# Kernel optimization log

Measured on AMD Instinct MI355X. Metric: run time of the kernel, lower is better.

## Reference

```python
import jax, jax.numpy as jnp
import numpy as np

B, L, D, H = 8, 1024, 512, 8
DH = D // H  # 64
EPS = 1e-5


def setup_inputs() -> dict:
    key = jax.random.key(0)
    ks = jax.random.split(key, 9)
    query = jax.random.normal(ks[0], (B, L, D), dtype=jnp.float32)
    key_t = jax.random.normal(ks[1], (B, L, D), dtype=jnp.float32)
    value = jax.random.normal(ks[2], (B, L, D), dtype=jnp.float32)
    attn_mask = jax.random.bernoulli(ks[3], 0.1, (B, L, L))
    softmax_mask = jax.random.bernoulli(ks[4], 0.1, (B, L, L))
    s = 1.0 / np.sqrt(D)
    Wq = jax.random.uniform(ks[5], (D, D), jnp.float32, -s, s)
    Wk = jax.random.uniform(ks[6], (D, D), jnp.float32, -s, s)
    Wv = jax.random.uniform(ks[7], (D, D), jnp.float32, -s, s)
    Wo = jax.random.uniform(ks[8], (D, D), jnp.float32, -s, s)
    return {"query": query, "key": key_t, "value": value,
            "attn_mask": attn_mask, "softmax_mask": softmax_mask,
            "Wq": Wq, "Wk": Wk, "Wv": Wv, "Wo": Wo}


def _split_heads(x):
    # [B, L, D] -> [B, H, L, DH]
    b, l, _ = x.shape
    return x.reshape(b, l, H, DH).transpose(0, 2, 1, 3)


def reference(query, key, value, attn_mask, softmax_mask, Wq, Wk, Wv, Wo):
    residual = query
    q = _split_heads(query @ Wq.T)   # [B,H,L,DH]
    k = _split_heads(key @ Wk.T)
    v = _split_heads(value @ Wv.T)
    scale = DH ** (-0.5)
    scores = jnp.einsum("bhqd,bhkd->bhqk", q, k) * scale
    scores = jnp.where(attn_mask[:, None], -jnp.inf, scores)
    attention = jax.nn.softmax(scores, axis=-1)
    attention = jnp.where(softmax_mask[:, None], 0.0, attention)
    # dropout p = 0.0 -> identity
    context = jnp.einsum("bhqk,bhkd->bhqd", attention, v)
    context = context.transpose(0, 2, 1, 3).reshape(query.shape[0], -1, D)
    output = context @ Wo.T
    x = residual + output
    mean = jnp.mean(x, axis=-1, keepdims=True)
    var = jnp.var(x, axis=-1, keepdims=True)
    out = (x - mean) * jax.lax.rsqrt(var + EPS)  # LayerNorm, no affine
    return out, attention
```

## Files before the change

### kernel.cpp

```cpp
#include <hip/hip_runtime.h>

#define BB 8
#define LL 1024
#define DD 512
#define HH 8

typedef __attribute__((ext_vector_type(8))) short bf16x8;
typedef __attribute__((ext_vector_type(4))) float f32x4;

__device__ __forceinline__ unsigned short f2bf(float f) {
    union { float f; unsigned u; } c; c.f = f;
    unsigned u = c.u + 0x7fffu + ((c.u >> 16) & 1u);
    return (unsigned short)(u >> 16);
}

template<bool F32SRC>
__device__ __forceinline__ uint4 ld8bf(const void* base, size_t idx) {
    if (F32SRC) {
        const float* p = (const float*)base + idx;
        const float4 a = *reinterpret_cast<const float4*>(p);
        const float4 b = *reinterpret_cast<const float4*>(p + 4);
        uint4 o;
        o.x = (unsigned)f2bf(a.x) | ((unsigned)f2bf(a.y) << 16);
        o.y = (unsigned)f2bf(a.z) | ((unsigned)f2bf(a.w) << 16);
        o.z = (unsigned)f2bf(b.x) | ((unsigned)f2bf(b.y) << 16);
        o.w = (unsigned)f2bf(b.z) | ((unsigned)f2bf(b.w) << 16);
        return o;
    } else {
        return *reinterpret_cast<const uint4*>((const unsigned short*)base + idx);
    }
}

__global__ __launch_bounds__(256) void maskpack_kernel(
    const int* __restrict__ am, const int* __restrict__ sm,
    unsigned* __restrict__ ab, unsigned* __restrict__ sb)
{
    const int4* src = reinterpret_cast<const int4*>(blockIdx.y ? sm : am);
    unsigned* dst   = blockIdx.y ? sb : ab;
    for (int g = blockIdx.x * 256 + threadIdx.x; g < 2097152; g += gridDim.x * 256) {
        const int4 x = src[g];
        unsigned nib = (unsigned)(x.x != 0) | ((unsigned)(x.y != 0) << 1)
                     | ((unsigned)(x.z != 0) << 2) | ((unsigned)(x.w != 0) << 3);
        unsigned word = nib << ((g & 7) * 4);
        word |= __shfl_xor(word, 1);
        word |= __shfl_xor(word, 2);
        word |= __shfl_xor(word, 4);
        if ((threadIdx.x & 7) == 0) dst[g >> 3] = word;
    }
}

template<bool OUTBF, bool AF32, bool WF32>
__device__ __forceinline__ void gemm_mfma_body(
    const void* __restrict__ Av, const void* __restrict__ Wv,
    void* __restrict__ Yv)
{
    __shared__ unsigned short As[128 * 40];
    __shared__ unsigned short Bs[128 * 40];
    const int t = threadIdx.x, w = t >> 6, lane = t & 63;
    const int ln15 = lane & 15, quad = lane >> 4;
    const int wm = w & 1, wn = w >> 1;
    const int m0 = blockIdx.y * 128, n0 = blockIdx.x * 128;
    f32x4 acc[4][4];
    #pragma unroll
    for (int i = 0; i < 4; i++)
        #pragma unroll
        for (int j = 0; j < 4; j++) acc[i][j] = (f32x4){0.f, 0.f, 0.f, 0.f};

    for (int k0 = 0; k0 < 512; k0 += 32) {
        uint4 ga[2], gb[2];
        #pragma unroll
        for (int i = 0; i < 2; i++) {
            const int u = t + i * 256, row = u >> 2, ch = (u & 3) * 8;
            ga[i] = ld8bf<AF32>(Av, (size_t)(m0 + row) * 512 + k0 + ch);
            gb[i] = ld8bf<WF32>(Wv, (size_t)(n0 + row) * 512 + k0 + ch);
        }
        if (k0) __syncthreads();
        #pragma unroll
        for (int i = 0; i < 2; i++) {
            const int u = t + i * 256, row = u >> 2, ch = (u & 3) * 8;
            *reinterpret_cast<uint4*>(&As[row * 40 + ch]) = ga[i];
            *reinterpret_cast<uint4*>(&Bs[row * 40 + ch]) = gb[i];
        }
        __syncthreads();
        bf16x8 af[4], bf_[4];
        #pragma unroll
        for (int s = 0; s < 4; s++) {
            af[s]  = *reinterpret_cast<const bf16x8*>(&As[(wm * 64 + s * 16 + ln15) * 40 + quad * 8]);
            bf_[s] = *reinterpret_cast<const bf16x8*>(&Bs[(wn * 64 + s * 16 + ln15) * 40 + quad * 8]);
        }
        #pragma unroll
        for (int sm_ = 0; sm_ < 4; sm_++)
            #pragma unroll
            for (int sn_ = 0; sn_ < 4; sn_++)
                acc[sm_][sn_] = __builtin_amdgcn_mfma_f32_16x16x32_bf16(
                    af[sm_], bf_[sn_], acc[sm_][sn_], 0, 0, 0);
    }
    #pragma unroll
    for (int sm_ = 0; sm_ < 4; sm_++)
        #pragma unroll
        for (int sn_ = 0; sn_ < 4; sn_++)
            #pragma unroll
            for (int r = 0; r < 4; r++) {
                const int row = m0 + wm * 64 + sm_ * 16 + quad * 4 + r;
                const int col = n0 + wn * 64 + sn_ * 16 + ln15;
                if (OUTBF)
                    ((unsigned short*)Yv)[(size_t)row * 512 + col] = f2bf(acc[sm_][sn_][r]);
                else
                    ((float*)Yv)[(size_t)row * 512 + col] = acc[sm_][sn_][r];
            }
}

__global__ __launch_bounds__(256) void gemm3_kernel(
    const float* a0, const float* a1, const float* a2,
    const float* w0, const float* w1, const float* w2,
    unsigned short* y0, unsigned short* y1, unsigned short* y2)
{
    const float *A, *W; unsigned short* Y;
    if (blockIdx.z == 0)      { A = a0; W = w0; Y = y0; }
    else if (blockIdx.z == 1) { A = a1; W = w1; Y = y1; }
    else                      { A = a2; W = w2; Y = y2; }
    gemm_mfma_body<true, true, true>(A, W, Y);
}

__global__ __launch_bounds__(256) void gemm1_kernel(
    const unsigned short* A, const float* W, float* Y)
{
    gemm_mfma_body<false, false, true>(A, W, Y);
}

__global__ __launch_bounds__(256) void vtrans_kernel(
    const unsigned short* __restrict__ Vb, unsigned short* __restrict__ Vt)
{
    __shared__ unsigned short tile[64 * 72];
    const int t = threadIdx.x;
    const int tt = blockIdx.x, h = blockIdx.y, b = blockIdx.z;
    #pragma unroll
    for (int i = 0; i < 2; i++) {
        const int u = t + i * 256, row = u >> 3, ch = (u & 7) * 8;
        *reinterpret_cast<uint4*>(&tile[row * 72 + ch]) =
            *reinterpret_cast<const uint4*>(&Vb[(size_t)(b * 1024 + tt * 64 + row) * 512 + h * 64 + ch]);
    }
    __syncthreads();
    #pragma unroll
    for (int i = 0; i < 2; i++) {
        const int u = t + i * 256, dh = u >> 3, ch = (u & 7) * 8;
        unsigned short r8[8];
        #pragma unroll
        for (int e = 0; e < 8; e++) r8[e] = tile[(ch + e) * 72 + dh];
        uint4 o;
        o.x = (unsigned)r8[0] | ((unsigned)r8[1] << 16);
        o.y = (unsigned)r8[2] | ((unsigned)r8[3] << 16);
        o.z = (unsigned)r8[4] | ((unsigned)r8[5] << 16);
        o.w = (unsigned)r8[6] | ((unsigned)r8[7] << 16);
        *reinterpret_cast<uint4*>(&Vt[(size_t)((b * 8 + h) * 64 + dh) * 1024 + tt * 64 + ch]) = o;
    }
}

__global__ __launch_bounds__(512) void fattn_kernel(
    const unsigned short* __restrict__ Qb, const unsigned short* __restrict__ Kb,
    const unsigned short* __restrict__ Vt,
    const unsigned* __restrict__ ab, const unsigned* __restrict__ sb,
    float* __restrict__ attn, unsigned short* __restrict__ CTX)
{
    __shared__ __align__(16) unsigned short Ks[2][64 * 72];
    __shared__ __align__(16) unsigned short Vs[2][64 * 72];
    __shared__ __align__(16) unsigned short Pt[8][16 * 72];
    const int t = threadIdx.x, w = t >> 6, lane = t & 63;
    const int ln15 = lane & 15, quad = lane >> 4;
    const int id = blockIdx.x;
    const int b = id & 7, slot = id >> 3;
    const int qt = slot & 7, h = slot >> 3;
    const int bh = b * 8 + h;
    const int qbase = qt * 128 + w * 16;

    const int srow = t >> 3, sch = (t & 7) * 8;
    const size_t kg = ((size_t)(b * 1024 + srow)) * 512 + h * 64 + sch;
    const size_t vg = ((size_t)(bh * 64 + srow)) * 1024 + sch;
    const int sidx = srow * 72 + sch;

    const size_t qoff = ((size_t)(b * 1024) + qbase + ln15) * 512 + h * 64 + quad * 8;
    const bf16x8 aq0 = *reinterpret_cast<const bf16x8*>(Qb + qoff);
    const bf16x8 aq1 = *reinterpret_cast<const bf16x8*>(Qb + qoff + 32);

    int mrow[4];
    #pragma unroll
    for (int r = 0; r < 4; r++)
        mrow[r] = (b * 1024 + qbase + quad * 4 + r) * 32;

    uint4 kr = *reinterpret_cast<const uint4*>(Kb + kg);
    *reinterpret_cast<uint4*>(&Ks[0][sidx]) = kr;
    __syncthreads();

    float l[4];
    #pragma unroll
    for (int r = 0; r < 4; r++) l[r] = 0.f;

    int cur = 0;
    for (int kt = 0; kt < 16; kt++) {
        if (kt < 15)
            kr = *reinterpret_cast<const uint4*>(Kb + kg + (size_t)(kt + 1) * 32768);
        f32x4 acc[4];
        #pragma unroll
        for (int sub = 0; sub < 4; sub++) {
            const bf16x8 bk0 = *reinterpret_cast<const bf16x8*>(&Ks[cur][(sub * 16 + ln15) * 72 + quad * 8]);
            const bf16x8 bk1 = *reinterpret_cast<const bf16x8*>(&Ks[cur][(sub * 16 + ln15) * 72 + quad * 8 + 32]);
            f32x4 c = __builtin_amdgcn_mfma_f32_16x16x32_bf16(aq0, bk0, (f32x4){0.f,0.f,0.f,0.f}, 0, 0, 0);
            acc[sub] = __builtin_amdgcn_mfma_f32_16x16x32_bf16(aq1, bk1, c, 0, 0, 0);
        }
        #pragma unroll
        for (int r = 0; r < 4; r++) {
            const unsigned w0 = ab[mrow[r] + kt * 2], w1 = ab[mrow[r] + kt * 2 + 1];
            #pragma unroll
            for (int sub = 0; sub < 4; sub++) {
                const int cb = sub * 16 + ln15;
                const unsigned msk = ((cb & 32 ? w1 : w0) >> (cb & 31)) & 1u;
                const float e = __expf(acc[sub][r] * 0.125f);
                l[r] += msk ? 0.f : e;
            }
        }
        if (kt < 15)
            *reinterpret_cast<uint4*>(&Ks[cur ^ 1][sidx]) = kr;
        __syncthreads();
        cur ^= 1;
    }

    kr = *reinterpret_cast<const uint4*>(Kb + kg);
    uint4 vr = *reinterpret_cast<const uint4*>(Vt + vg);
    float invl[4];
    #pragma unroll
    for (int r = 0; r < 4; r++) {
        #pragma unroll
        for (int off = 1; off < 16; off <<= 1) l[r] += __shfl_xor(l[r], off);
        invl[r] = 1.f / l[r];
    }
    *reinterpret_cast<uint4*>(&Ks[0][sidx]) = kr;
    *reinterpret_cast<uint4*>(&Vs[0][sidx]) = vr;
    __syncthreads();

    float* ap[4];
    #pragma unroll
    for (int r = 0; r < 4; r++)
        ap[r] = attn + ((size_t)bh * 1024 + qbase + quad * 4 + r) * 1024 + ln15;

    f32x4 o[4];
    #pragma unroll
    for (int sn = 0; sn < 4; sn++) o[sn] = (f32x4){0.f, 0.f, 0.f, 0.f};
    unsigned short* Pw = Pt[w];

    cur = 0;
    for (int kt = 0; kt < 16; kt++) {
        if (kt < 15) {
            kr = *reinterpret_cast<const uint4*>(Kb + kg + (size_t)(kt + 1) * 32768);
            vr = *reinterpret_cast<const uint4*>(Vt + vg + (size_t)(kt + 1) * 64);
        }
        f32x4 acc[4];
        #pragma unroll
        for (int sub = 0; sub < 4; sub++) {
            const bf16x8 bk0 = *reinterpret_cast<const bf16x8*>(&Ks[cur][(sub * 16 + ln15) * 72 + quad * 8]);
            const bf16x8 bk1 = *reinterpret_cast<const bf16x8*>(&Ks[cur][(sub * 16 + ln15) * 72 + quad * 8 + 32]);
            f32x4 c = __builtin_amdgcn_mfma_f32_16x16x32_bf16(aq0, bk0, (f32x4){0.f,0.f,0.f,0.f}, 0, 0, 0);
            acc[sub] = __builtin_amdgcn_mfma_f32_16x16x32_bf16(aq1, bk1, c, 0, 0, 0);
        }
        #pragma unroll
        for (int r = 0; r < 4; r++) {
            const unsigned a0 = ab[mrow[r] + kt * 2], a1 = ab[mrow[r] + kt * 2 + 1];
            const unsigned s0 = sb[mrow[r] + kt * 2], s1 = sb[mrow[r] + kt * 2 + 1];
            #pragma unroll
            for (int sub = 0; sub < 4; sub++) {
                const int cb = sub * 16 + ln15;
                const unsigned amsk = ((cb & 32 ? a1 : a0) >> (cb & 31)) & 1u;
                const unsigned smsk = ((cb & 32 ? s1 : s0) >> (cb & 31)) & 1u;
                float a = __expf(acc[sub][r] * 0.125f) * invl[r];
                a = amsk ? 0.f : a;
                a = smsk ? 0.f : a;
                ap[r][kt * 64 + sub * 16] = a;
                Pw[(quad * 4 + r) * 72 + cb] = f2bf(a);
            }
        }
        const bf16x8 pa0 = *reinterpret_cast<const bf16x8*>(&Pw[ln15 * 72 + quad * 8]);
        const bf16x8 pa1 = *reinterpret_cast<const bf16x8*>(&Pw[ln15 * 72 + 32 + quad * 8]);
        #pragma unroll
        for (int sn = 0; sn < 4; sn++) {
            const bf16x8 vb0 = *reinterpret_cast<const bf16x8*>(&Vs[cur][(sn * 16 + ln15) * 72 + quad * 8]);
            const bf16x8 vb1 = *reinterpret_cast<const bf16x8*>(&Vs[cur][(sn * 16 + ln15) * 72 + quad * 8 + 32]);
            o[sn] = __builtin_amdgcn_mfma_f32_16x16x32_bf16(pa0, vb0, o[sn], 0, 0, 0);
            o[sn] = __builtin_amdgcn_mfma_f32_16x16x32_bf16(pa1, vb1, o[sn], 0, 0, 0);
        }
        if (kt < 15) {
            *reinterpret_cast<uint4*>(&Ks[cur ^ 1][sidx]) = kr;
            *reinterpret_cast<uint4*>(&Vs[cur ^ 1][sidx]) = vr;
        }
        __syncthreads();
        cur ^= 1;
    }
    #pragma unroll
    for (int sn = 0; sn < 4; sn++)
        #pragma unroll
        for (int r = 0; r < 4; r++)
            CTX[((size_t)(b * 1024) + qbase + quad * 4 + r) * 512 + h * 64 + sn * 16 + ln15] =
                f2bf(o[sn][r]);
}

__global__ __launch_bounds__(256) void ln_kernel(
    const float* __restrict__ X, const float* __restrict__ R,
    float* __restrict__ out)
{
    __shared__ float rs[4], rq[4];
    const int r = blockIdx.x, t = threadIdx.x;
    const float2 xv = *reinterpret_cast<const float2*>(&X[(size_t)r * 512 + 2 * t]);
    const float2 rv = *reinterpret_cast<const float2*>(&R[(size_t)r * 512 + 2 * t]);
    const float x0 = xv.x + rv.x, x1 = xv.y + rv.y;
    float s = x0 + x1, q = x0 * x0 + x1 * x1;
    #pragma unroll
    for (int off = 32; off > 0; off >>= 1) { s += __shfl_xor(s, off); q += __shfl_xor(q, off); }
    if ((t & 63) == 0) { rs[t >> 6] = s; rq[t >> 6] = q; }
    __syncthreads();
    s = rs[0] + rs[1] + rs[2] + rs[3];
    q = rq[0] + rq[1] + rq[2] + rq[3];
    const float mean = s * (1.f / 512.f);
    const float var  = q * (1.f / 512.f) - mean * mean;
    const float rstd = rsqrtf(var + 1e-5f);
    float2 o;
    o.x = (x0 - mean) * rstd;
    o.y = (x1 - mean) * rstd;
    *reinterpret_cast<float2*>(&out[(size_t)r * 512 + 2 * t]) = o;
}

extern "C" void kernel_launch(void* const* d_in, const int* in_sizes, int n_in,
                              void* d_out, int out_size, void* d_ws, size_t ws_size,
                              hipStream_t stream)
{
    const float* q  = (const float*)d_in[0];
    const float* k  = (const float*)d_in[1];
    const float* v  = (const float*)d_in[2];
    const int*   am = (const int*)d_in[3];
    const int*   sm = (const int*)d_in[4];
    const float* wq = (const float*)d_in[5];
    const float* wk = (const float*)d_in[6];
    const float* wv = (const float*)d_in[7];
    const float* wo = (const float*)d_in[8];

    float* out  = (float*)d_out;
    float* attn = out + (size_t)BB * LL * DD;

    unsigned char* W = (unsigned char*)d_ws;
    unsigned short* Vt   = (unsigned short*)(W + 0);
    unsigned short* CTXb = (unsigned short*)(W + 8388608);
    unsigned*       ab   = (unsigned*)      (W + 27262976);
    unsigned*       sb   = (unsigned*)      (W + 28311552);
    unsigned short* Qbf  = (unsigned short*)(W + 29360128);
    unsigned short* Kbf  = (unsigned short*)(W + 37748736);
    unsigned short* Vbf  = (unsigned short*)(W + 46137344);
    float*          X2f  = (float*)(W + 29360128);

    maskpack_kernel<<<dim3(2048, 2, 1), 256, 0, stream>>>(am, sm, ab, sb);
    gemm3_kernel<<<dim3(4, 64, 3), 256, 0, stream>>>(q, k, v,
        wq, wk, wv, Qbf, Kbf, Vbf);
    vtrans_kernel<<<dim3(16, 8, 8), 256, 0, stream>>>(Vbf, Vt);
    fattn_kernel<<<dim3(512, 1, 1), 512, 0, stream>>>(Qbf, Kbf, Vt, ab, sb, attn, CTXb);
    gemm1_kernel<<<dim3(4, 64, 1), 256, 0, stream>>>(CTXb, wo, X2f);
    ln_kernel<<<dim3(8192, 1, 1), 256, 0, stream>>>(X2f, q, out);
}
```

Measured before the change: 498.4 us.

## Fuse output projection with residual LayerNorm and double-buffer GEMM shared tiles

Replaces the separate output-projection GEMM and LayerNorm kernels with one kernel. Each block computes full 512-wide rows for 32 tokens, adds the residual and normalizes in registers, so the fp32 intermediate is never written to or read back from global memory. It also adds register-prefetched double buffering of LDS tiles in the shared GEMM body used by the QKV projections. The trade-off is that every block reloads and converts all of Wo from fp32, and fewer, larger blocks are launched.

After: 494.1 us. No clear change (-0.9%).

```diff
diff --git a/kernel.cpp b/kernel.cpp
--- a/kernel.cpp
+++ b/kernel.cpp
@@ -54,8 +54,8 @@
     const void* __restrict__ Av, const void* __restrict__ Wv,
     void* __restrict__ Yv)
 {
-    __shared__ unsigned short As[128 * 40];
-    __shared__ unsigned short Bs[128 * 40];
+    __shared__ unsigned short As[2][128 * 40];
+    __shared__ unsigned short Bs[2][128 * 40];
     const int t = threadIdx.x, w = t >> 6, lane = t & 63;
     const int ln15 = lane & 15, quad = lane >> 4;
     const int wm = w & 1, wn = w >> 1;
@@ -66,27 +66,36 @@
         #pragma unroll
         for (int j = 0; j < 4; j++) acc[i][j] = (f32x4){0.f, 0.f, 0.f, 0.f};
 
+    uint4 ga[2], gb[2];
+    #pragma unroll
+    for (int i = 0; i < 2; i++) {
+        const int u = t + i * 256, r_ = u >> 2, c_ = (u & 3) * 8;
+        ga[i] = ld8bf<AF32>(Av, (size_t)(m0 + r_) * 512 + c_);
+        gb[i] = ld8bf<WF32>(Wv, (size_t)(n0 + r_) * 512 + c_);
+    }
+    #pragma unroll
+    for (int i = 0; i < 2; i++) {
+        const int u = t + i * 256, r_ = u >> 2, c_ = (u & 3) * 8;
+        *reinterpret_cast<uint4*>(&As[0][r_ * 40 + c_]) = ga[i];
+        *reinterpret_cast<uint4*>(&Bs[0][r_ * 40 + c_]) = gb[i];
+    }
+    __syncthreads();
+
+    int cur = 0;
     for (int k0 = 0; k0 < 512; k0 += 32) {
-        uint4 ga[2], gb[2];
-        #pragma unroll
-        for (int i = 0; i < 2; i++) {
-            const int u = t + i * 256, row = u >> 2, ch = (u & 3) * 8;
-            ga[i] = ld8bf<AF32>(Av, (size_t)(m0 + row) * 512 + k0 + ch);
-            gb[i] = ld8bf<WF32>(Wv, (size_t)(n0 + row) * 512 + k0 + ch);
-        }
-        if (k0) __syncthreads();
-        #pragma unroll
-        for (int i = 0; i < 2; i++) {
-            const int u = t + i * 256, row = u >> 2, ch = (u & 3) * 8;
-            *reinterpret_cast<uint4*>(&As[row * 40 + ch]) = ga[i];
-            *reinterpret_cast<uint4*>(&Bs[row * 40 + ch]) = gb[i];
-        }
-        __syncthreads();
+        if (k0 < 480) {
+            #pragma unroll
+            for (int i = 0; i < 2; i++) {
+                const int u = t + i * 256, r_ = u >> 2, c_ = (u & 3) * 8;
+                ga[i] = ld8bf<AF32>(Av, (size_t)(m0 + r_) * 512 + k0 + 32 + c_);
+                gb[i] = ld8bf<WF32>(Wv, (size_t)(n0 + r_) * 512 + k0 + 32 + c_);
+            }
+        }
         bf16x8 af[4], bf_[4];
         #pragma unroll
         for (int s = 0; s < 4; s++) {
-            af[s]  = *reinterpret_cast<const bf16x8*>(&As[(wm * 64 + s * 16 + ln15) * 40 + quad * 8]);
-            bf_[s] = *reinterpret_cast<const bf16x8*>(&Bs[(wn * 64 + s * 16 + ln15) * 40 + quad * 8]);
+            af[s]  = *reinterpret_cast<const bf16x8*>(&As[cur][(wm * 64 + s * 16 + ln15) * 40 + quad * 8]);
+            bf_[s] = *reinterpret_cast<const bf16x8*>(&Bs[cur][(wn * 64 + s * 16 + ln15) * 40 + quad * 8]);
         }
         #pragma unroll
         for (int sm_ = 0; sm_ < 4; sm_++)
@@ -94,6 +103,16 @@
             for (int sn_ = 0; sn_ < 4; sn_++)
                 acc[sm_][sn_] = __builtin_amdgcn_mfma_f32_16x16x32_bf16(
                     af[sm_], bf_[sn_], acc[sm_][sn_], 0, 0, 0);
+        if (k0 < 480) {
+            #pragma unroll
+            for (int i = 0; i < 2; i++) {
+                const int u = t + i * 256, r_ = u >> 2, c_ = (u & 3) * 8;
+                *reinterpret_cast<uint4*>(&As[cur ^ 1][r_ * 40 + c_]) = ga[i];
+                *reinterpret_cast<uint4*>(&Bs[cur ^ 1][r_ * 40 + c_]) = gb[i];
+            }
+        }
+        __syncthreads();
+        cur ^= 1;
     }
     #pragma unroll
     for (int sm_ = 0; sm_ < 4; sm_++)
@@ -122,10 +141,104 @@
     gemm_mfma_body<true, true, true>(A, W, Y);
 }
 
-__global__ __launch_bounds__(256) void gemm1_kernel(
-    const unsigned short* A, const float* W, float* Y)
-{
-    gemm_mfma_body<false, false, true>(A, W, Y);
+__global__ __launch_bounds__(512) void gemmln_kernel(
+    const unsigned short* __restrict__ A,
+    const float* __restrict__ Wo,
+    const float* __restrict__ R,
+    float* __restrict__ out)
+{
+    __shared__ unsigned short As[32 * 40];
+    __shared__ unsigned short Bs[512 * 40];
+    __shared__ float2 sums[32][8];
+    __shared__ float2 mv[32];
+    const int t = threadIdx.x, w = t >> 6, lane = t & 63;
+    const int ln15 = lane & 15, quad = lane >> 4;
+    const int m0 = blockIdx.x * 32;
+
+    f32x4 acc[2][4];
+    #pragma unroll
+    for (int i = 0; i < 2; i++)
+        #pragma unroll
+        for (int j = 0; j < 4; j++) acc[i][j] = (f32x4){0.f, 0.f, 0.f, 0.f};
+
+    for (int k0 = 0; k0 < 512; k0 += 32) {
+        uint4 gav; uint4 gbv[4];
+        if (t < 128) {
+            const int r_ = t >> 2, c_ = (t & 3) * 8;
+            gav = ld8bf<false>(A, (size_t)(m0 + r_) * 512 + k0 + c_);
+        }
+        #pragma unroll
+        for (int i = 0; i < 4; i++) {
+            const int u = t + i * 512, r_ = u >> 2, c_ = (u & 3) * 8;
+            gbv[i] = ld8bf<true>(Wo, (size_t)r_ * 512 + k0 + c_);
+        }
+        if (k0) __syncthreads();
+        if (t < 128) {
+            const int r_ = t >> 2, c_ = (t & 3) * 8;
+            *reinterpret_cast<uint4*>(&As[r_ * 40 + c_]) = gav;
+        }
+        #pragma unroll
+        for (int i = 0; i < 4; i++) {
+            const int u = t + i * 512, r_ = u >> 2, c_ = (u & 3) * 8;
+            *reinterpret_cast<uint4*>(&Bs[r_ * 40 + c_]) = gbv[i];
+        }
+        __syncthreads();
+        bf16x8 af[2], bf_[4];
+        #pragma unroll
+        for (int s = 0; s < 2; s++)
+            af[s] = *reinterpret_cast<const bf16x8*>(&As[(s * 16 + ln15) * 40 + quad * 8]);
+        #pragma unroll
+        for (int s = 0; s < 4; s++)
+            bf_[s] = *reinterpret_cast<const bf16x8*>(&Bs[(w * 64 + s * 16 + ln15) * 40 + quad * 8]);
+        #pragma unroll
+        for (int sm_ = 0; sm_ < 2; sm_++)
+            #pragma unroll
+            for (int sn_ = 0; sn_ < 4; sn_++)
+                acc[sm_][sn_] = __builtin_amdgcn_mfma_f32_16x16x32_bf16(
+                    af[sm_], bf_[sn_], acc[sm_][sn_], 0, 0, 0);
+    }
+
+    #pragma unroll
+    for (int sm_ = 0; sm_ < 2; sm_++)
+        #pragma unroll
+        for (int r = 0; r < 4; r++) {
+            const int row = sm_ * 16 + quad * 4 + r;
+            float s_ = 0.f, q_ = 0.f;
+            #pragma unroll
+            for (int sn_ = 0; sn_ < 4; sn_++) {
+                const float val = acc[sm_][sn_][r]
+                    + R[(size_t)(m0 + row) * 512 + w * 64 + sn_ * 16 + ln15];
+                acc[sm_][sn_][r] = val;
+                s_ += val; q_ += val * val;
+            }
+            #pragma unroll
+            for (int off = 1; off < 16; off <<= 1) {
+                s_ += __shfl_xor(s_, off);
+                q_ += __shfl_xor(q_, off);
+            }
+            if (ln15 == 0) sums[row][w] = make_float2(s_, q_);
+        }
+    __syncthreads();
+    if (t < 32) {
+        float s_ = 0.f, q_ = 0.f;
+        #pragma unroll
+        for (int i = 0; i < 8; i++) { s_ += sums[t][i].x; q_ += sums[t][i].y; }
+        const float mean = s_ * (1.f / 512.f);
+        const float var  = q_ * (1.f / 512.f) - mean * mean;
+        mv[t] = make_float2(mean, rsqrtf(var + 1e-5f));
+    }
+    __syncthreads();
+    #pragma unroll
+    for (int sm_ = 0; sm_ < 2; sm_++)
+        #pragma unroll
+        for (int r = 0; r < 4; r++) {
+            const int row = sm_ * 16 + quad * 4 + r;
+            const float2 m_ = mv[row];
+            #pragma unroll
+            for (int sn_ = 0; sn_ < 4; sn_++)
+                out[(size_t)(m0 + row) * 512 + w * 64 + sn_ * 16 + ln15] =
+                    (acc[sm_][sn_][r] - m_.x) * m_.y;
+        }
 }
 
 __global__ __launch_bounds__(256) void vtrans_kernel(
@@ -301,31 +414,6 @@
                 f2bf(o[sn][r]);
 }
 
-__global__ __launch_bounds__(256) void ln_kernel(
-    const float* __restrict__ X, const float* __restrict__ R,
-    float* __restrict__ out)
-{
-    __shared__ float rs[4], rq[4];
-    const int r = blockIdx.x, t = threadIdx.x;
-    const float2 xv = *reinterpret_cast<const float2*>(&X[(size_t)r * 512 + 2 * t]);
-    const float2 rv = *reinterpret_cast<const float2*>(&R[(size_t)r * 512 + 2 * t]);
-    const float x0 = xv.x + rv.x, x1 = xv.y + rv.y;
-    float s = x0 + x1, q = x0 * x0 + x1 * x1;
-    #pragma unroll
-    for (int off = 32; off > 0; off >>= 1) { s += __shfl_xor(s, off); q += __shfl_xor(q, off); }
-    if ((t & 63) == 0) { rs[t >> 6] = s; rq[t >> 6] = q; }
-    __syncthreads();
-    s = rs[0] + rs[1] + rs[2] + rs[3];
-    q = rq[0] + rq[1] + rq[2] + rq[3];
-    const float mean = s * (1.f / 512.f);
-    const float var  = q * (1.f / 512.f) - mean * mean;
-    const float rstd = rsqrtf(var + 1e-5f);
-    float2 o;
-    o.x = (x0 - mean) * rstd;
-    o.y = (x1 - mean) * rstd;
-    *reinterpret_cast<float2*>(&out[(size_t)r * 512 + 2 * t]) = o;
-}
-
 extern "C" void kernel_launch(void* const* d_in, const int* in_sizes, int n_in,
                               void* d_out, int out_size, void* d_ws, size_t ws_size,
                               hipStream_t stream)
@@ -351,13 +439,11 @@
     unsigned short* Qbf  = (unsigned short*)(W + 29360128);
     unsigned short* Kbf  = (unsigned short*)(W + 37748736);
     unsigned short* Vbf  = (unsigned short*)(W + 46137344);
-    float*          X2f  = (float*)(W + 29360128);
 
     maskpack_kernel<<<dim3(2048, 2, 1), 256, 0, stream>>>(am, sm, ab, sb);
     gemm3_kernel<<<dim3(4, 64, 3), 256, 0, stream>>>(q, k, v,
         wq, wk, wv, Qbf, Kbf, Vbf);
     vtrans_kernel<<<dim3(16, 8, 8), 256, 0, stream>>>(Vbf, Vt);
     fattn_kernel<<<dim3(512, 1, 1), 512, 0, stream>>>(Qbf, Kbf, Vt, ab, sb, attn, CTXb);
-    gemm1_kernel<<<dim3(4, 64, 1), 256, 0, stream>>>(CTXb, wo, X2f);
-    ln_kernel<<<dim3(8192, 1, 1), 256, 0, stream>>>(X2f, q, out);
-}
+    gemmln_kernel<<<dim3(256, 1, 1), 512, 0, stream>>>(CTXb, wo, q, out);
+}
```
